# Performance work log

Measured on AMD Instinct MI355X. Metric: run time of the kernel, lower is better.

The kernel has to match this reference:

```python
import jax, jax.numpy as jnp
import numpy as np

B, T, F = 8, 1024, 80
STACK, STRIDE = 4, 4          # encoder.embed.right_context+1, subsampling_rate
G, E, C = 4, 16, 8192         # num_codebooks, embedding_dim, num_embeddings
DENC = 512                    # encoder.output_size()
TS = (T - STACK) // STRIDE + 1
FREG = 0.01                   # features_regularization_weight
EPS = 1e-5


def setup_inputs() -> dict:
    key = jax.random.key(0)
    ks = jax.random.split(key, 12)
    feats = jax.random.normal(ks[0], (B, T, F), jnp.float32)
    feats_lengths = jax.random.randint(ks[1], (B,), T // 2, T + 1, jnp.int32)
    # span masks (True = masked), mask_length=10 spans so full subsample windows get masked
    n_spans, ML = 16, 10
    starts = jax.random.randint(ks[2], (B, n_spans), 0, T - ML)
    pos = starts[:, :, None] + jnp.arange(ML)  # [B, n_spans, ML]
    masks = jnp.zeros((B, T), bool).at[jnp.arange(B)[:, None, None], pos].set(True)
    mask_emb = 0.1 * jax.random.normal(ks[3], (1, 1, F), jnp.float32)
    signal_mean = 0.1 * jax.random.normal(ks[4], (F,), jnp.float32)
    signal_istd = jax.random.uniform(ks[5], (F,), jnp.float32, 0.5, 1.5)
    projection = jax.random.normal(ks[6], (STACK * F, G * E), jnp.float32) * np.sqrt(2.0 / (STACK * F + G * E))
    embeddings = jax.random.normal(ks[7], (C, G, E), jnp.float32)
    encoder_top_n_out = 0.02 * jax.random.normal(ks[8], (G, DENC, C), jnp.float32)
    encoder_top_n_out_bias = jnp.zeros((G, C), jnp.float32)
    encoder_out = jax.random.normal(ks[9], (B, TS, DENC), jnp.float32)
    return {"feats": feats, "feats_lengths": feats_lengths, "masks": masks,
            "mask_emb": mask_emb, "signal_mean": signal_mean, "signal_istd": signal_istd,
            "projection": projection, "embeddings": embeddings,
            "encoder_top_n_out": encoder_top_n_out,
            "encoder_top_n_out_bias": encoder_top_n_out_bias,
            "encoder_out": encoder_out}


def _quantize_codes(latent, codebook):
    # latent: [N, G*E] -> codes [N, G]; codebook: [C, G, E]
    lat = latent.reshape(latent.shape[0], G, E)
    dist = (jnp.sum(lat ** 2, -1, keepdims=True)
            - 2.0 * jnp.einsum('ngd,cgd->ngc', lat, codebook)
            + jnp.sum(codebook ** 2, -1).T[None])  # [N, G, C]
    return jnp.argmin(dist, axis=-1)


def reference(feats, feats_lengths, masks, mask_emb, signal_mean, signal_istd,
              projection, embeddings, encoder_top_n_out, encoder_top_n_out_bias,
              encoder_out):
    # global CMVN
    xs = (feats - signal_mean) * signal_istd  # [B, T, F]
    features_pen = jnp.mean(xs ** 2)
    # masked signal (fed to the delegated encoder in the original; encoder_out stands in)
    _masked_xs = jnp.where(masks[:, :, None], mask_emb, xs)
    # unfold windows
    widx = jnp.arange(TS)[:, None] * STRIDE + jnp.arange(STACK)  # [TS, STACK]
    code_ids_mask = jnp.all(masks[:, widx], axis=2)  # [B, TS] (torch.min over bool window)
    stacked = xs[:, widx].reshape(B, TS, STACK * F)  # _stack_features on unmasked input
    # LayerNorm (no affine)
    mu = jnp.mean(stacked, -1, keepdims=True)
    var = jnp.var(stacked, -1, keepdims=True)
    normed = (stacked - mu) / jnp.sqrt(var + EPS)
    proj = normed @ projection  # [B, TS, G*E]
    target = _quantize_codes(proj.reshape(B * TS, G * E), embeddings).reshape(B, TS, G)
    # encoder output mask after subsampling
    lens_sub = jnp.maximum((feats_lengths - STACK) // STRIDE + 1, 0)
    out_mask = jnp.arange(TS)[None, :] < lens_sub[:, None]
    m = (out_mask & code_ids_mask).astype(jnp.float32)  # [B, TS]
    # big matmul: [B,1,TS,DENC] x [1,G,DENC,C] + bias -> [B,G,TS,C]
    logits = jnp.einsum('btd,gdc->bgtc', encoder_out, encoder_top_n_out) \
             + encoder_top_n_out_bias[None, :, None, :]
    logp = jax.nn.log_softmax(logits, axis=-1).transpose(0, 2, 1, 3)  # [B, TS, G, C]
    per = -jnp.take_along_axis(logp, target[..., None], axis=-1)[..., 0]  # [B, TS, G]
    denom = jnp.sum(m) + 1e-5
    loss = jnp.sum(per * m[:, :, None]) / (denom * G) + FREG * features_pen
    num_codes = jnp.sum(m) * G
    corr = (jnp.argmax(logits, -1).transpose(0, 2, 1) == target)
    codes_acc = jnp.sum(corr * m[:, :, None]) / num_codes
    vals = (target * m[:, :, None].astype(target.dtype)).reshape(-1)
    uniq_num_codes = jnp.zeros((C,), bool).at[vals].set(True).sum()
    return (loss, codes_acc, features_pen, num_codes, uniq_num_codes)
```

## Files before the change

kernel.cpp:

```cpp
#include <hip/hip_runtime.h>
#include <hip/hip_bf16.h>
#include <math.h>
#include <stddef.h>

#define NB 8
#define NT 1024
#define NF 80
#define NSTACK 4
#define NSTRIDE 4
#define NG 4
#define NE 16
#define NC 8192
#define ND 512
#define NTS 256
#define NP (NB*NTS)
#define SFD (NSTACK*NF)
#define FREG 0.01f
#define LNEPS 1e-5f

#define TCC 1024
#define CPT 4
#define PCH 16
#define PB 16

#define ROWS_MAX 2176
#define ROWCH 144
#define MT 9
#define QCH 16
#define QY 32
#define CT 128
#define QS 8
#define STG16H 1152
#define WST 1024

typedef __attribute__((ext_vector_type(8))) short short8;
typedef __attribute__((ext_vector_type(4))) float f32x4;

struct Ws {
  float penSum;
  unsigned int nA;
  unsigned int maskIsInt;
  unsigned int pad1;
  unsigned long long amax[NP*NG];
  float sumExp[NP*NG];
  float tLogit[NP*NG];
  int   targets[NP*NG];
  int   activeList[NP];
  float penPart[256];
  unsigned long long aminS[NP*NG*QS];
  float lat[NP][64];
  unsigned short aHiT[(size_t)(ND/8)*ROWS_MAX*8];
  unsigned short aLoT[(size_t)(ND/8)*ROWS_MAX*8];
  float part_se[NG][ROWS_MAX][CT];
  unsigned long long part_mx[NG][ROWS_MAX][CT];
};

__device__ inline unsigned short bf16_rne(float x) {
  unsigned u = __float_as_uint(x);
  unsigned r = u + 0x7FFFu + ((u >> 16) & 1u);
  return (unsigned short)(r >> 16);
}
__device__ inline unsigned fkey_asc(float d) {
  unsigned u = __float_as_uint(d);
  return (u & 0x80000000u) ? ~u : (u | 0x80000000u);
}
__device__ __forceinline__ void gload_lds16(const void* g, void* l) {
  __builtin_amdgcn_global_load_lds(
      (const __attribute__((address_space(1))) void*)g,
      (__attribute__((address_space(3))) void*)l, 16, 0, 0);
}

__global__ __launch_bounds__(256) void k_prologue(
    const float* __restrict__ feats, const float* __restrict__ mean,
    const float* __restrict__ istd, const unsigned char* __restrict__ m8,
    const int* __restrict__ lens, int doClear, Ws* ws) {
  const int tid = threadIdx.x;
  if (doClear) ws->aminS[(size_t)blockIdx.x*256 + tid] = ~0ull;

  const int N4 = NB*NT*NF/4;
  float s = 0.f;
  for (int i = blockIdx.x*256 + tid; i < N4; i += gridDim.x*256) {
    float4 v = reinterpret_cast<const float4*>(feats)[i];
    int f0 = (i*4) % NF;
    float x0 = (v.x - mean[f0+0]) * istd[f0+0];
    float x1 = (v.y - mean[f0+1]) * istd[f0+1];
    float x2 = (v.z - mean[f0+2]) * istd[f0+2];
    float x3 = (v.w - mean[f0+3]) * istd[f0+3];
    s += x0*x0 + x1*x1 + x2*x2 + x3*x3;
  }
  for (int o = 32; o; o >>= 1) s += __shfl_down(s, o);
  __shared__ float pr[4];
  if ((tid & 63) == 0) pr[tid >> 6] = s;
  __syncthreads();
  if (tid == 0) ws->penPart[blockIdx.x] = pr[0]+pr[1]+pr[2]+pr[3];

  if (blockIdx.x == 0) {
    __shared__ unsigned flag;
    __shared__ int sCnt[256];
    if (tid == 0) flag = 0;
    __syncthreads();
    unsigned nz = 0;
    int base = tid * 32;
    for (int i = base; i < base + 32; ++i)
      if ((i & 3) && m8[i]) nz = 1;
    if (nz) atomicOr(&flag, 1u);
    __syncthreads();
    bool isInt = (flag == 0);
    const int* m32 = (const int*)m8;

    unsigned bits = 0;
    int cnt = 0;
    #pragma unroll
    for (int j = 0; j < 8; ++j) {
      int p = tid*8 + j;
      int b = p >> 8, ts = p & (NTS-1);
      int t0 = b*NT + ts*NSTRIDE;
      bool allm;
      if (isInt) allm = m32[t0] && m32[t0+1] && m32[t0+2] && m32[t0+3];
      else       allm = m8[t0] && m8[t0+1] && m8[t0+2] && m8[t0+3];
      int ls = (lens[b] - NSTACK)/NSTRIDE + 1;
      if (ls < 0) ls = 0;
      bool act = allm && (ts < ls);
      bits |= (unsigned)act << j;
      cnt += act;
    }
    sCnt[tid] = cnt;
    __syncthreads();
    #pragma unroll
    for (int off = 1; off < 256; off <<= 1) {
      int v = (tid >= off) ? sCnt[tid - off] : 0;
      __syncthreads();
      sCnt[tid] += v;
      __syncthreads();
    }
    int wr = sCnt[tid] - cnt;
    #pragma unroll
    for (int j = 0; j < 8; ++j) {
      if (bits & (1u << j)) ws->activeList[wr++] = tid*8 + j;
    }
    if (tid == 255) ws->nA = (unsigned)sCnt[255];
  }
}

__global__ __launch_bounds__(256) void k_latprep(
    const float* __restrict__ feats, const float* __restrict__ mean,
    const float* __restrict__ istd, const float* __restrict__ projw,
    const float* __restrict__ enc, Ws* ws) {
  int nA = (int)ws->nA;
  int ai = blockIdx.x;
  int limit = ((nA + ROWCH - 1) / ROWCH) * ROWCH;
  int tid = threadIdx.x;

  if (ai >= nA) {
    if (ai < limit && tid < 64) {
      short8 z;
      #pragma unroll
      for (int j = 0; j < 8; ++j) z[j] = 0;
      *reinterpret_cast<short8*>(ws->aHiT + ((size_t)tid*ROWS_MAX + ai)*8) = z;
      *reinterpret_cast<short8*>(ws->aLoT + ((size_t)tid*ROWS_MAX + ai)*8) = z;
    }
    return;
  }

  int p = ws->activeList[ai];
  if (tid < 64) {
    const float* src = enc + (size_t)p*ND + tid*8;
    float4 x0 = *reinterpret_cast<const float4*>(src);
    float4 x1 = *reinterpret_cast<const float4*>(src + 4);
    float xv[8] = {x0.x, x0.y, x0.z, x0.w, x1.x, x1.y, x1.z, x1.w};
    short8 h, l;
    #pragma unroll
    for (int j = 0; j < 8; ++j) {
      unsigned short hi = bf16_rne(xv[j]);
      float rem = xv[j] - __uint_as_float((unsigned)hi << 16);
      h[j] = (short)hi;
      l[j] = (short)bf16_rne(rem);
    }
    *reinterpret_cast<short8*>(ws->aHiT + ((size_t)tid*ROWS_MAX + ai)*8) = h;
    *reinterpret_cast<short8*>(ws->aLoT + ((size_t)tid*ROWS_MAX + ai)*8) = l;
  }

  int b = p >> 8, ts = p & (NTS-1);
  __shared__ float sN[SFD];
  __shared__ float sPart[4*64];
  __shared__ float rS[4], rQ[4];

  for (int j = tid; j < SFD; j += 256) {
    int k = j / NF, f = j - k*NF;
    sN[j] = (feats[((size_t)b*NT + ts*NSTRIDE + k)*NF + f] - mean[f]) * istd[f];
  }
  __syncthreads();
  float s = 0.f, q = 0.f;
  for (int j = tid; j < SFD; j += 256) { float x = sN[j]; s += x; q += x*x; }
  for (int o = 32; o; o >>= 1) { s += __shfl_down(s, o); q += __shfl_down(q, o); }
  if ((tid & 63) == 0) { rS[tid>>6] = s; rQ[tid>>6] = q; }
  __syncthreads();
  float mu  = (rS[0]+rS[1]+rS[2]+rS[3]) * (1.f/SFD);
  float var = (rQ[0]+rQ[1]+rQ[2]+rQ[3]) * (1.f/SFD) - mu*mu;
  float inv = rsqrtf(var + LNEPS);
  for (int j = tid; j < SFD; j += 256) sN[j] = (sN[j]-mu)*inv;
  __syncthreads();
  {
    int j = tid & 63, part = tid >> 6;
    float a = 0.f;
    int i0 = part*80;
    for (int i = i0; i < i0+80; ++i) a = fmaf(sN[i], projw[i*64 + j], a);
    sPart[part*64 + j] = a;
  }
  __syncthreads();
  if (tid < 64)
    ws->lat[ai][tid] = sPart[tid] + sPart[64+tid] + sPart[128+tid] + sPart[192+tid];
}

__global__ __launch_bounds__(256) void k_qdist(const float* __restrict__ emb, Ws* ws) {
  int nA = (int)ws->nA;
  if (nA == 0) return;
  int tid = threadIdx.x;
  int g = tid >> 6, lane = tid & 63;
  int c = blockIdx.x * 64 + lane;
  int per = (nA + QY - 1) / QY;
  int a0 = blockIdx.y * per;
  int a1 = min(nA, a0 + per);
  int slot = blockIdx.x & (QS-1);

  const float4* e4 = reinterpret_cast<const float4*>(emb + ((size_t)c*NG + g)*NE);
  float4 b0 = e4[0], b1 = e4[1], b2 = e4[2], b3 = e4[3];
  float n2 = b0.x*b0.x + b0.y*b0.y + b0.z*b0.z + b0.w*b0.w
           + b1.x*b1.x + b1.y*b1.y + b1.z*b1.z + b1.w*b1.w
           + b2.x*b2.x + b2.y*b2.y + b2.z*b2.z + b2.w*b2.w
           + b3.x*b3.x + b3.y*b3.y + b3.z*b3.z + b3.w*b3.w;

  __shared__ float sL[QCH][64];
  for (int base = a0; base < a1; base += QCH) {
    int cnt = min(QCH, a1 - base);
    __syncthreads();
    for (int i = tid; i < cnt*64; i += 256)
      (&sL[0][0])[i] = (&ws->lat[0][0])[(size_t)(base + (i >> 6))*64 + (i & 63)];
    __syncthreads();
    for (int i = 0; i < cnt; ++i) {
      const float* lp = &sL[i][g*NE];
      float dot = lp[0]*b0.x + lp[1]*b0.y + lp[2]*b0.z + lp[3]*b0.w
                + lp[4]*b1.x + lp[5]*b1.y + lp[6]*b1.z + lp[7]*b1.w
                + lp[8]*b2.x + lp[9]*b2.y + lp[10]*b2.z + lp[11]*b2.w
                + lp[12]*b3.x + lp[13]*b3.y + lp[14]*b3.z + lp[15]*b3.w;
      float d = n2 - 2.f*dot;
      float mv = d; int mc = c;
      #pragma unroll
      for (int off = 32; off; off >>= 1) {
        float ov = __shfl_xor(mv, off);
        int   oc = __shfl_xor(mc, off);
        if (ov < mv || (ov == mv && oc < mc)) { mv = ov; mc = oc; }
      }
      if (lane == 0) {
        unsigned long long key =
            ((unsigned long long)fkey_asc(mv) << 32) | (unsigned)mc;
        atomicMin(&ws->aminS[(size_t)((base + i)*NG + g)*QS + slot], key);
      }
    }
  }
}

__global__ __launch_bounds__(512, 4) void k_logits_mfma(
    const float* __restrict__ W, const float* __restrict__ bias, Ws* ws) {
  const int nA = (int)ws->nA;
  if (nA == 0) return;
  const int nCh = (nA + ROWCH - 1) / ROWCH;
  const int tid = threadIdx.x;
  const int wave = tid >> 6, lane = tid & 63;
  const int sub = wave & 3, kh = wave >> 2;
  const int g = blockIdx.y;
  const int c0blk = blockIdx.x * 64;
  const int c0w = c0blk + sub * 16;
  const int lo16 = lane & 15, hi4 = lane >> 4;
  const int cOut0 = c0w + hi4*4;
  float bv[4];
  #pragma unroll
  for (int v = 0; v < 4; ++v) bv[v] = bias[g*NC + cOut0 + v];

  __shared__ __align__(16) unsigned char smem[53248];
  unsigned short* sH = (unsigned short*)smem;
  unsigned short* sLb = (unsigned short*)(smem + 18432);
  float* sW = (float*)(smem + 36864);
  f32x4 (*sAcc)[MT][64] = (f32x4 (*)[MT][64])smem;
  float (*sEs)[ROWCH] = (float (*)[ROWCH])(smem + 36864);
  unsigned long long (*sMx)[ROWCH] =
      (unsigned long long (*)[ROWCH])(smem + 36864 + 2560);

  const int krow0 = tid >> 4,       woff0 = (tid & 15) * 4;
  const int krow1 = (tid+512) >> 4, woff1 = ((tid+512) & 15) * 4;
  const size_t wk0 = (size_t)((krow0 < 32) ? krow0 : 224 + krow0);
  const size_t wk1 = (size_t)((krow1 < 32) ? krow1 : 224 + krow1);
  const float* __restrict__ wG = W + ((size_t)g*ND)*NC + c0blk;

  const int wRd = (kh*32 + hi4*8)*64 + sub*16 + lo16;

  for (int ch = 0; ch < nCh; ++ch) {
    const int r0 = ch * ROWCH;

    size_t off0, off1, off2; bool v2;
    {
      int t = tid;
      int part = t/144, row = t - part*144;
      off0 = ((size_t)((part>>2)*32 + (part&3))*ROWS_MAX + r0 + row)*8;
      t = tid + 512;
      part = t/144; row = t - part*144;
      off1 = ((size_t)((part>>2)*32 + (part&3))*ROWS_MAX + r0 + row)*8;
      t = tid + 1024;
      v2 = (t < STG16H);
      part = t/144; row = t - part*144;
      off2 = v2 ? ((size_t)((part>>2)*32 + (part&3))*ROWS_MAX + r0 + row)*8 : 0;
    }

    f32x4 acc[MT];
    #pragma unroll
    for (int mt = 0; mt < MT; ++mt) acc[mt] = (f32x4){0.f, 0.f, 0.f, 0.f};

    gload_lds16(ws->aHiT + off0, sH + (size_t)tid*8);
    gload_lds16(ws->aHiT + off1, sH + (size_t)(tid + 512)*8);
    if (v2) gload_lds16(ws->aHiT + off2, sH + (size_t)(tid + 1024)*8);
    gload_lds16(wG + wk0*NC + woff0, sW + (size_t)tid*4);
    gload_lds16(wG + wk1*NC + woff1, sW + (size_t)(tid + 512)*4);
    __syncthreads();

    #pragma unroll 1
    for (int step = 0; step < 8; ++step) {
      const size_t kAdv = (size_t)step*4*ROWS_MAX*8;
      gload_lds16(ws->aLoT + off0 + kAdv, sLb + (size_t)tid*8);
      gload_lds16(ws->aLoT + off1 + kAdv, sLb + (size_t)(tid + 512)*8);
      if (v2) gload_lds16(ws->aLoT + off2 + kAdv, sLb + (size_t)(tid + 1024)*8);
      float wv[8];
      #pragma unroll
      for (int j = 0; j < 8; ++j) wv[j] = sW[wRd + j*64];
      short8 whi, wlo;
      #pragma unroll
      for (int j = 0; j < 8; ++j) {
        unsigned short h = bf16_rne(wv[j]);
        float rem = wv[j] - __uint_as_float((unsigned)h << 16);
        whi[j] = (short)h;
        wlo[j] = (short)bf16_rne(rem);
      }
      const unsigned short* bpH = sH + ((size_t)((kh*4 + hi4)*144 + lo16))*8;
      #pragma unroll
      for (int mt = 0; mt < MT; ++mt) {
        short8 bh = *reinterpret_cast<const short8*>(bpH + mt*128);
        acc[mt] = __builtin_amdgcn_mfma_f32_16x16x32_bf16(whi, bh, acc[mt], 0, 0, 0);
        acc[mt] = __builtin_amdgcn_mfma_f32_16x16x32_bf16(wlo, bh, acc[mt], 0, 0, 0);
      }
      __syncthreads();
      if (step < 7) {
        const size_t kAdv2 = kAdv + (size_t)4*ROWS_MAX*8;
        gload_lds16(ws->aHiT + off0 + kAdv2, sH + (size_t)tid*8);
        gload_lds16(ws->aHiT + off1 + kAdv2, sH + (size_t)(tid + 512)*8);
        if (v2) gload_lds16(ws->aHiT + off2 + kAdv2, sH + (size_t)(tid + 1024)*8);
        const size_t wAdv = (size_t)(step+1)*32*NC;
        gload_lds16(wG + (wk0*NC + wAdv) + woff0, sW + (size_t)tid*4);
        gload_lds16(wG + (wk1*NC + wAdv) + woff1, sW + (size_t)(tid + 512)*4);
      }
      const unsigned short* bpL = sLb + ((size_t)((kh*4 + hi4)*144 + lo16))*8;
      #pragma unroll
      for (int mt = 0; mt < MT; ++mt) {
        short8 bl = *reinterpret_cast<const short8*>(bpL + mt*128);
        acc[mt] = __builtin_amdgcn_mfma_f32_16x16x32_bf16(whi, bl, acc[mt], 0, 0, 0);
      }
      __syncthreads();
    }

    if (kh == 1) {
      #pragma unroll
      for (int mt = 0; mt < MT; ++mt) sAcc[sub][mt][lane] = acc[mt];
    }
    __syncthreads();

    if (kh == 0) {
      #pragma unroll
      for (int mt = 0; mt < MT; ++mt) {
        const int row = r0 + mt*16 + lo16;
        int tgt = -1;
        if (row < nA) {
          const unsigned long long* ap = ws->aminS + (size_t)(row*NG + g)*QS;
          unsigned long long m = ap[0];
          #pragma unroll
          for (int s2 = 1; s2 < QS; ++s2) {
            unsigned long long v = ap[s2];
            if (v < m) m = v;
          }
          tgt = (int)(unsigned)(m & 0xFFFFFFFFull);
          if (blockIdx.x == 0 && wave == 0 && hi4 == 0)
            ws->targets[row*NG + g] = tgt;
        }
        f32x4 oth = sAcc[sub][mt][lane];
        float lv[4];
        #pragma unroll
        for (int v = 0; v < 4; ++v) lv[v] = (acc[mt][v] + oth[v]) + bv[v];
        #pragma unroll
        for (int v = 0; v < 4; ++v)
          if (tgt == cOut0 + v) ws->tLogit[row*NG + g] = lv[v];
        float es = expf(lv[0]) + expf(lv[1]) + expf(lv[2]) + expf(lv[3]);
        float mv = lv[0]; int mi = cOut0;
        if (lv[1] > mv) { mv = lv[1]; mi = cOut0+1; }
        if (lv[2] > mv) { mv = lv[2]; mi = cOut0+2; }
        if (lv[3] > mv) { mv = lv[3]; mi = cOut0+3; }
        #pragma unroll
        for (int off = 16; off <= 32; off <<= 1) {
          es += __shfl_xor(es, off);
          float ov = __shfl_xor(mv, off);
          int   oi = __shfl_xor(mi, off);
          if (ov > mv || (ov == mv && oi < mi)) { mv = ov; mi = oi; }
        }
        if (hi4 == 0) {
          sEs[sub][mt*16 + lo16] = es;
          unsigned key = __float_as_uint(mv);
          key = (key & 0x80000000u) ? ~key : (key | 0x80000000u);
          sMx[sub][mt*16 + lo16] = ((unsigned long long)key << 32)
                                 | (unsigned long long)(0xFFFFFFFFu - (unsigned)mi);
        }
      }
    }
    __syncthreads();
    if (tid < ROWCH) {
      float e = sEs[0][tid] + sEs[1][tid] + sEs[2][tid] + sEs[3][tid];
      unsigned long long m0 = sMx[0][tid], m1 = sMx[1][tid];
      unsigned long long m2 = sMx[2][tid], m3 = sMx[3][tid];
      unsigned long long ma = m0 > m1 ? m0 : m1;
      unsigned long long mb = m2 > m3 ? m2 : m3;
      unsigned long long mx = ma > mb ? ma : mb;
      int grow = r0 + tid;
      ws->part_se[g][grow][blockIdx.x] = e;
      ws->part_mx[g][grow][blockIdx.x] = mx;
    }
    __syncthreads();
  }
}

__global__ __launch_bounds__(256) void k_red_l(Ws* ws) {
  int nA = (int)ws->nA;
  int pair = blockIdx.x*4 + (threadIdx.x >> 6);
  int lane = threadIdx.x & 63;
  int row = pair >> 2, g = pair & 3;
  if (row >= nA) return;
  float e = ws->part_se[g][row][lane] + ws->part_se[g][row][lane + 64];
  unsigned long long a = ws->part_mx[g][row][lane];
  unsigned long long b = ws->part_mx[g][row][lane + 64];
  unsigned long long mx = a > b ? a : b;
  #pragma unroll
  for (int off = 32; off; off >>= 1) {
    e += __shfl_xor(e, off);
    unsigned long long o = __shfl_xor(mx, off);
    if (o > mx) mx = o;
  }
  if (lane == 0) {
    ws->sumExp[row*NG + g] = e;
    ws->amax[row*NG + g] = mx;
  }
}

__global__ __launch_bounds__(256) void k_quant(
    const float* __restrict__ feats, const float* __restrict__ mean,
    const float* __restrict__ istd, const float* __restrict__ projw,
    const float* __restrict__ emb, Ws* ws) {
  if (blockIdx.x >= ws->nA) return;
  int ai = blockIdx.x;
  int p = ws->activeList[ai];
  int b = p >> 8, ts = p & (NTS-1);
  int tid = threadIdx.x;
  __shared__ float sN[SFD];
  __shared__ float sPart[4*64];
  __shared__ float sLat[NG*NE];
  __shared__ float sRedS[256];
  __shared__ int   sRedC[256];
  __shared__ float rS[4], rQ[4];
  __shared__ int   sTgt[NG];

  for (int j = tid; j < SFD; j += 256) {
    int k = j / NF, f = j - k*NF;
    sN[j] = (feats[((size_t)b*NT + ts*NSTRIDE + k)*NF + f] - mean[f]) * istd[f];
  }
  __syncthreads();
  float s = 0.f, q = 0.f;
  for (int j = tid; j < SFD; j += 256) { float x = sN[j]; s += x; q += x*x; }
  for (int o = 32; o; o >>= 1) { s += __shfl_down(s, o); q += __shfl_down(q, o); }
  if ((tid & 63) == 0) { rS[tid>>6] = s; rQ[tid>>6] = q; }
  __syncthreads();
  float mu  = (rS[0]+rS[1]+rS[2]+rS[3]) * (1.f/SFD);
  float var = (rQ[0]+rQ[1]+rQ[2]+rQ[3]) * (1.f/SFD) - mu*mu;
  float inv = rsqrtf(var + LNEPS);
  for (int j = tid; j < SFD; j += 256) sN[j] = (sN[j]-mu)*inv;
  __syncthreads();
  {
    int j = tid & 63, part = tid >> 6;
    float a = 0.f;
    int i0 = part*80;
    for (int i = i0; i < i0+80; ++i) a = fmaf(sN[i], projw[i*64 + j], a);
    sPart[part*64 + j] = a;
  }
  __syncthreads();
  if (tid < 64) sLat[tid] = sPart[tid] + sPart[64+tid] + sPart[128+tid] + sPart[192+tid];
  __syncthreads();

  for (int gg = 0; gg < NG; ++gg) {
    float lg[NE];
    #pragma unroll
    for (int e = 0; e < NE; ++e) lg[e] = sLat[gg*NE + e];
    float best = 3.4e38f; int bc = NC;
    for (int c = tid; c < NC; c += 256) {
      const float4* cb4 = reinterpret_cast<const float4*>(emb + ((size_t)c*NG + gg)*NE);
      float4 a0 = cb4[0], a1 = cb4[1], a2 = cb4[2], a3 = cb4[3];
      float dot = 0.f, n2 = 0.f;
      dot = fmaf(lg[0],  a0.x, dot); n2 = fmaf(a0.x, a0.x, n2);
      dot = fmaf(lg[1],  a0.y, dot); n2 = fmaf(a0.y, a0.y, n2);
      dot = fmaf(lg[2],  a0.z, dot); n2 = fmaf(a0.z, a0.z, n2);
      dot = fmaf(lg[3],  a0.w, dot); n2 = fmaf(a0.w, a0.w, n2);
      dot = fmaf(lg[4],  a1.x, dot); n2 = fmaf(a1.x, a1.x, n2);
      dot = fmaf(lg[5],  a1.y, dot); n2 = fmaf(a1.y, a1.y, n2);
      dot = fmaf(lg[6],  a1.z, dot); n2 = fmaf(a1.z, a1.z, n2);
      dot = fmaf(lg[7],  a1.w, dot); n2 = fmaf(a1.w, a1.w, n2);
      dot = fmaf(lg[8],  a2.x, dot); n2 = fmaf(a2.x, a2.x, n2);
      dot = fmaf(lg[9],  a2.y, dot); n2 = fmaf(a2.y, a2.y, n2);
      dot = fmaf(lg[10], a2.z, dot); n2 = fmaf(a2.z, a2.z, n2);
      dot = fmaf(lg[11], a2.w, dot); n2 = fmaf(a2.w, a2.w, n2);
      dot = fmaf(lg[12], a3.x, dot); n2 = fmaf(a3.x, a3.x, n2);
      dot = fmaf(lg[13], a3.y, dot); n2 = fmaf(a3.y, a3.y, n2);
      dot = fmaf(lg[14], a3.z, dot); n2 = fmaf(a3.z, a3.z, n2);
      dot = fmaf(lg[15], a3.w, dot); n2 = fmaf(a3.w, a3.w, n2);
      float sc = n2 - 2.f*dot;
      if (sc < best) { best = sc; bc = c; }
    }
    sRedS[tid] = best; sRedC[tid] = bc;
    __syncthreads();
    for (int off = 128; off; off >>= 1) {
      if (tid < off) {
        float os = sRedS[tid+off]; int oc = sRedC[tid+off];
        if (os < sRedS[tid] || (os == sRedS[tid] && oc < sRedC[tid])) {
          sRedS[tid] = os; sRedC[tid] = oc;
        }
      }
      __syncthreads();
    }
    if (tid == 0) sTgt[gg] = sRedC[0];
    __syncthreads();
  }
  if (tid < NG) ws->targets[ai*NG + tid] = sTgt[tid];
}

__global__ __launch_bounds__(256) void k_logits(
    const float* __restrict__ W, const float* __restrict__ bias,
    const float* __restrict__ enc, Ws* ws) {
  const int nA = (int)ws->nA;
  if (nA == 0) return;
  const int nCh = (nA + PCH - 1) / PCH;
  const int g = blockIdx.y;
  const int cbase = blockIdx.x * TCC + threadIdx.x * CPT;
  const float* __restrict__ Wg = W + (size_t)g*ND*NC;
  const float b0 = bias[g*NC + cbase + 0];
  const float b1 = bias[g*NC + cbase + 1];
  const float b2 = bias[g*NC + cbase + 2];
  const float b3 = bias[g*NC + cbase + 3];
  __shared__ float4 sEnc[PCH][ND/4];
  __shared__ int sP[PCH];

  for (int ch = blockIdx.z; ch < nCh; ch += PB) {
    if (threadIdx.x < PCH) {
      int ai = ch*PCH + threadIdx.x;
      sP[threadIdx.x] = (ai < nA) ? ws->activeList[ai] : -1;
    }
    __syncthreads();
    for (int i = threadIdx.x; i < PCH*(ND/4); i += 256) {
      int qq = i >> 7, r = i & 127;
      int p = sP[qq];
      sEnc[qq][r] = (p >= 0) ? reinterpret_cast<const float4*>(enc)[p*(ND/4) + r]
                             : make_float4(0.f, 0.f, 0.f, 0.f);
    }
    __syncthreads();

    float acc[PCH][CPT];
    #pragma unroll
    for (int qq = 0; qq < PCH; ++qq)
      #pragma unroll
      for (int j = 0; j < CPT; ++j) acc[qq][j] = 0.f;
    for (int d = 0; d < ND; d += 4) {
      const float* wp = Wg + (size_t)d*NC + cbase;
      float4 w0 = *reinterpret_cast<const float4*>(wp);
      float4 w1 = *reinterpret_cast<const float4*>(wp + NC);
      float4 w2 = *reinterpret_cast<const float4*>(wp + 2*NC);
      float4 w3 = *reinterpret_cast<const float4*>(wp + 3*NC);
      int dq = d >> 2;
      #pragma unroll
      for (int qq = 0; qq < PCH; ++qq) {
        float4 e = sEnc[qq][dq];
        acc[qq][0] = fmaf(e.x, w0.x, acc[qq][0]);
        acc[qq][1] = fmaf(e.x, w0.y, acc[qq][1]);
        acc[qq][2] = fmaf(e.x, w0.z, acc[qq][2]);
        acc[qq][3] = fmaf(e.x, w0.w, acc[qq][3]);
        acc[qq][0] = fmaf(e.y, w1.x, acc[qq][0]);
        acc[qq][1] = fmaf(e.y, w1.y, acc[qq][1]);
        acc[qq][2] = fmaf(e.y, w1.z, acc[qq][2]);
        acc[qq][3] = fmaf(e.y, w1.w, acc[qq][3]);
        acc[qq][0] = fmaf(e.z, w2.x, acc[qq][0]);
        acc[qq][1] = fmaf(e.z, w2.y, acc[qq][1]);
        acc[qq][2] = fmaf(e.z, w2.z, acc[qq][2]);
        acc[qq][3] = fmaf(e.z, w2.w, acc[qq][3]);
        acc[qq][0] = fmaf(e.w, w3.x, acc[qq][0]);
        acc[qq][1] = fmaf(e.w, w3.y, acc[qq][1]);
        acc[qq][2] = fmaf(e.w, w3.z, acc[qq][2]);
        acc[qq][3] = fmaf(e.w, w3.w, acc[qq][3]);
      }
    }

    #pragma unroll
    for (int qq = 0; qq < PCH; ++qq) {
      int ai = ch*PCH + qq;
      if (ai < nA) {
        float l0 = acc[qq][0] + b0;
        float l1 = acc[qq][1] + b1;
        float l2 = acc[qq][2] + b2;
        float l3 = acc[qq][3] + b3;
        int tgt = ws->targets[ai*NG + g];
        if ((unsigned)(tgt - cbase) < (unsigned)CPT) {
          float tv = (tgt == cbase) ? l0 : (tgt == cbase+1) ? l1
                   : (tgt == cbase+2) ? l2 : l3;
          ws->tLogit[ai*NG + g] = tv;
        }
        float es = expf(l0) + expf(l1) + expf(l2) + expf(l3);
        float mv = l0; int mi = cbase;
        if (l1 > mv) { mv = l1; mi = cbase+1; }
        if (l2 > mv) { mv = l2; mi = cbase+2; }
        if (l3 > mv) { mv = l3; mi = cbase+3; }
        for (int o = 32; o; o >>= 1) {
          es += __shfl_down(es, o);
          float ov = __shfl_down(mv, o);
          int   oi = __shfl_down(mi, o);
          if (ov > mv || (ov == mv && oi < mi)) { mv = ov; mi = oi; }
        }
        if ((threadIdx.x & 63) == 0) {
          atomicAdd(&ws->sumExp[ai*NG + g], es);
          unsigned key = __float_as_uint(mv);
          key = (key & 0x80000000u) ? ~key : (key | 0x80000000u);
          unsigned long long pk =
              ((unsigned long long)key << 32) |
              (unsigned long long)(0xFFFFFFFFu - (unsigned)mi);
          atomicMax(&ws->amax[ai*NG + g], pk);
        }
      }
    }
    __syncthreads();
  }
}

__global__ __launch_bounds__(256) void k_final(Ws* ws, float* __restrict__ out) {
  int tid = threadIdx.x;
  int nA = (int)ws->nA;
  __shared__ unsigned sbm[NC/32];
  sbm[tid] = 0u;
  __syncthreads();

  float sumPer = 0.f, sumCorr = 0.f;
  for (int i = tid; i < nA*NG; i += 256) {
    int tgt = ws->targets[i];
    sumPer += logf(ws->sumExp[i]) - ws->tLogit[i];
    unsigned long long pk = ws->amax[i];
    int mi = (int)(0xFFFFFFFFu - (unsigned)(pk & 0xFFFFFFFFull));
    if (mi == tgt) sumCorr += 1.f;
    atomicOr(&sbm[tgt >> 5], 1u << (tgt & 31));
  }
  __syncthreads();
  unsigned w = sbm[tid];
  if (tid == 0 && nA < NP) w |= 1u;
  int uniq = __popc(w);
  float pen1 = ws->penPart[tid];

  __shared__ float rs[4], rc[4], rp[4]; __shared__ int ru[4];
  float s1 = sumPer, s2 = sumCorr, s4 = pen1; int s3 = uniq;
  for (int o = 32; o; o >>= 1) {
    s1 += __shfl_down(s1, o);
    s2 += __shfl_down(s2, o);
    s3 += __shfl_down(s3, o);
    s4 += __shfl_down(s4, o);
  }
  if ((tid & 63) == 0) { rs[tid>>6] = s1; rc[tid>>6] = s2; ru[tid>>6] = s3; rp[tid>>6] = s4; }
  __syncthreads();
  if (tid == 0) {
    float sp = rs[0]+rs[1]+rs[2]+rs[3];
    float sc = rc[0]+rc[1]+rc[2]+rc[3];
    int   un = ru[0]+ru[1]+ru[2]+ru[3];
    float ps = rp[0]+rp[1]+rp[2]+rp[3];
    float pen   = ps / (float)(NB*NT*NF);
    float denom = (float)nA + 1e-5f;
    float nc    = (float)(nA * NG);
    out[0] = sp / (denom * (float)NG) + FREG * pen;
    out[1] = sc / nc;
    out[2] = pen;
    out[3] = nc;
    out[4] = (float)un;
  }
}

extern "C" void kernel_launch(void* const* d_in, const int* in_sizes, int n_in,
                              void* d_out, int out_size, void* d_ws, size_t ws_size,
                              hipStream_t stream) {
  const float* feats = (const float*)d_in[0];
  const int*   lens  = (const int*)d_in[1];
  const unsigned char* masks = (const unsigned char*)d_in[2];
  const float* mean  = (const float*)d_in[4];
  const float* istd  = (const float*)d_in[5];
  const float* projw = (const float*)d_in[6];
  const float* emb   = (const float*)d_in[7];
  const float* W     = (const float*)d_in[8];
  const float* bias  = (const float*)d_in[9];
  const float* enc   = (const float*)d_in[10];
  Ws* ws = (Ws*)d_ws;
  float* out = (float*)d_out;

  bool big = ws_size >= sizeof(Ws);
  if (big) {
    k_prologue<<<256, 256, 0, stream>>>(feats, mean, istd, masks, lens, 1, ws);
    k_latprep<<<ROWS_MAX, 256, 0, stream>>>(feats, mean, istd, projw, enc, ws);
    k_qdist<<<dim3(NC/64, QY), 256, 0, stream>>>(emb, ws);
    k_logits_mfma<<<dim3(CT, NG), 512, 0, stream>>>(W, bias, ws);
    k_red_l<<<NP, 256, 0, stream>>>(ws);
  } else {
    size_t zr = offsetof(Ws, aminS);
    hipMemsetAsync(d_ws, 0, ws_size < zr ? ws_size : zr, stream);
    k_prologue<<<256, 256, 0, stream>>>(feats, mean, istd, masks, lens, 0, ws);
    k_quant<<<NP, 256, 0, stream>>>(feats, mean, istd, projw, emb, ws);
    k_logits<<<dim3(NC/TCC, NG, PB), 256, 0, stream>>>(W, bias, enc, ws);
  }
  k_final<<<1, 256, 0, stream>>>(ws, out);
}
```

Measured before the change: 75.14 us.

## Fuse row reduction and final loss into logits kernel via last-block atomics

Removes the separate k_red_l and k_final launches on the big-workspace path. The last logits block finishing each codebook group, found with an atomic counter, reduces the partial sum-exp and max values for that group. The last group to finish then computes the final loss, accuracy, penalty and unique-code outputs. This saves two kernel launches and their gaps, but puts the reduction on a few serial blocks and depends on threadfence and atomic-counter ordering, with counters reset in the prologue.

```diff
diff --git a/kernel.cpp b/kernel.cpp
--- a/kernel.cpp
+++ b/kernel.cpp
@@ -31,7 +31,6 @@
 #define CT 128
 #define QS 8
 #define STG16H 1152
-#define WST 1024
 
 typedef __attribute__((ext_vector_type(8))) short short8;
 typedef __attribute__((ext_vector_type(4))) float f32x4;
@@ -47,6 +46,9 @@
   int   targets[NP*NG];
   int   activeList[NP];
   float penPart[256];
+  unsigned int redCnt[NG];
+  unsigned int finCnt;
+  unsigned int pad2[3];
   unsigned long long aminS[NP*NG*QS];
   float lat[NP][64];
   unsigned short aHiT[(size_t)(ND/8)*ROWS_MAX*8];
@@ -95,6 +97,11 @@
   if (tid == 0) ws->penPart[blockIdx.x] = pr[0]+pr[1]+pr[2]+pr[3];
 
   if (blockIdx.x == 0) {
+    if (tid == 0) {
+      ws->redCnt[0] = 0u; ws->redCnt[1] = 0u;
+      ws->redCnt[2] = 0u; ws->redCnt[3] = 0u;
+      ws->finCnt = 0u;
+    }
     __shared__ unsigned flag;
     __shared__ int sCnt[256];
     if (tid == 0) flag = 0;
@@ -261,7 +268,8 @@
 }
 
 __global__ __launch_bounds__(512, 4) void k_logits_mfma(
-    const float* __restrict__ W, const float* __restrict__ bias, Ws* ws) {
+    const float* __restrict__ W, const float* __restrict__ bias, Ws* ws,
+    float* __restrict__ out) {
   const int nA = (int)ws->nA;
   if (nA == 0) return;
   const int nCh = (nA + ROWCH - 1) / ROWCH;
@@ -278,6 +286,7 @@
   for (int v = 0; v < 4; ++v) bv[v] = bias[g*NC + cOut0 + v];
 
   __shared__ __align__(16) unsigned char smem[53248];
+  __shared__ unsigned sFlag, sFin;
   unsigned short* sH = (unsigned short*)smem;
   unsigned short* sLb = (unsigned short*)(smem + 18432);
   float* sW = (float*)(smem + 36864);
@@ -291,7 +300,6 @@
   const size_t wk0 = (size_t)((krow0 < 32) ? krow0 : 224 + krow0);
   const size_t wk1 = (size_t)((krow1 < 32) ? krow1 : 224 + krow1);
   const float* __restrict__ wG = W + ((size_t)g*ND)*NC + c0blk;
-
   const int wRd = (kh*32 + hi4*8)*64 + sub*16 + lo16;
 
   for (int ch = 0; ch < nCh; ++ch) {
@@ -430,27 +438,86 @@
     }
     __syncthreads();
   }
-}
-
-__global__ __launch_bounds__(256) void k_red_l(Ws* ws) {
-  int nA = (int)ws->nA;
-  int pair = blockIdx.x*4 + (threadIdx.x >> 6);
-  int lane = threadIdx.x & 63;
-  int row = pair >> 2, g = pair & 3;
-  if (row >= nA) return;
-  float e = ws->part_se[g][row][lane] + ws->part_se[g][row][lane + 64];
-  unsigned long long a = ws->part_mx[g][row][lane];
-  unsigned long long b = ws->part_mx[g][row][lane + 64];
-  unsigned long long mx = a > b ? a : b;
-  #pragma unroll
-  for (int off = 32; off; off >>= 1) {
-    e += __shfl_xor(e, off);
-    unsigned long long o = __shfl_xor(mx, off);
-    if (o > mx) mx = o;
-  }
-  if (lane == 0) {
-    ws->sumExp[row*NG + g] = e;
-    ws->amax[row*NG + g] = mx;
+
+  if (tid == 0) {
+    __threadfence();
+    sFlag = atomicAdd(&ws->redCnt[g], 1u);
+  }
+  __syncthreads();
+  if (sFlag != CT-1) return;
+  __threadfence();
+
+  for (int row = wave; row < nA; row += 8) {
+    float e = ws->part_se[g][row][lane] + ws->part_se[g][row][lane + 64];
+    unsigned long long a = ws->part_mx[g][row][lane];
+    unsigned long long b = ws->part_mx[g][row][lane + 64];
+    unsigned long long mx = a > b ? a : b;
+    #pragma unroll
+    for (int off = 32; off; off >>= 1) {
+      e += __shfl_xor(e, off);
+      unsigned long long o = __shfl_xor(mx, off);
+      if (o > mx) mx = o;
+    }
+    if (lane == 0) {
+      ws->sumExp[row*NG + g] = e;
+      ws->amax[row*NG + g] = mx;
+    }
+  }
+
+  if (tid == 0) {
+    __threadfence();
+    sFin = atomicAdd(&ws->finCnt, 1u);
+  }
+  __syncthreads();
+  if (sFin != NG-1) return;
+  __threadfence();
+
+  {
+    unsigned* sbm = (unsigned*)smem;
+    float* rS1 = (float*)(smem + 2048);
+    float* rS2 = rS1 + 8;
+    float* rS4 = rS2 + 8;
+    int*   rS3 = (int*)(rS4 + 8);
+    if (tid < 256) sbm[tid] = 0u;
+    __syncthreads();
+    float sumPer = 0.f, sumCorr = 0.f;
+    for (int i = tid; i < nA*NG; i += 512) {
+      int tgt = ws->targets[i];
+      sumPer += logf(ws->sumExp[i]) - ws->tLogit[i];
+      unsigned long long pk = ws->amax[i];
+      int mi = (int)(0xFFFFFFFFu - (unsigned)(pk & 0xFFFFFFFFull));
+      if (mi == tgt) sumCorr += 1.f;
+      atomicOr(&sbm[tgt >> 5], 1u << (tgt & 31));
+    }
+    float pen1 = (tid < 256) ? ws->penPart[tid] : 0.f;
+    __syncthreads();
+    unsigned wbits = (tid < 256) ? sbm[tid] : 0u;
+    if (tid == 0 && nA < NP) wbits |= 1u;
+    int uniq = __popc(wbits);
+    float s1 = sumPer, s2 = sumCorr, s4 = pen1; int s3 = uniq;
+    for (int o = 32; o; o >>= 1) {
+      s1 += __shfl_down(s1, o);
+      s2 += __shfl_down(s2, o);
+      s3 += __shfl_down(s3, o);
+      s4 += __shfl_down(s4, o);
+    }
+    if (lane == 0) { rS1[wave] = s1; rS2[wave] = s2; rS3[wave] = s3; rS4[wave] = s4; }
+    __syncthreads();
+    if (tid == 0) {
+      float sp = 0.f, sc = 0.f, ps = 0.f; int un = 0;
+      #pragma unroll
+      for (int wv = 0; wv < 8; ++wv) {
+        sp += rS1[wv]; sc += rS2[wv]; un += rS3[wv]; ps += rS4[wv];
+      }
+      float pen   = ps / (float)(NB*NT*NF);
+      float denom = (float)nA + 1e-5f;
+      float nc    = (float)(nA * NG);
+      out[0] = sp / (denom * (float)NG) + FREG * pen;
+      out[1] = sc / nc;
+      out[2] = pen;
+      out[3] = nc;
+      out[4] = (float)un;
+    }
   }
 }
 
@@ -715,14 +782,13 @@
     k_prologue<<<256, 256, 0, stream>>>(feats, mean, istd, masks, lens, 1, ws);
     k_latprep<<<ROWS_MAX, 256, 0, stream>>>(feats, mean, istd, projw, enc, ws);
     k_qdist<<<dim3(NC/64, QY), 256, 0, stream>>>(emb, ws);
-    k_logits_mfma<<<dim3(CT, NG), 512, 0, stream>>>(W, bias, ws);
-    k_red_l<<<NP, 256, 0, stream>>>(ws);
+    k_logits_mfma<<<dim3(CT, NG), 512, 0, stream>>>(W, bias, ws, out);
   } else {
     size_t zr = offsetof(Ws, aminS);
     hipMemsetAsync(d_ws, 0, ws_size < zr ? ws_size : zr, stream);
     k_prologue<<<256, 256, 0, stream>>>(feats, mean, istd, masks, lens, 0, ws);
     k_quant<<<NP, 256, 0, stream>>>(feats, mean, istd, projw, emb, ws);
     k_logits<<<dim3(NC/TCC, NG, PB), 256, 0, stream>>>(W, bias, enc, ws);
-  }
-  k_final<<<1, 256, 0, stream>>>(ws, out);
-}
+    k_final<<<1, 256, 0, stream>>>(ws, out);
+  }
+}
```

After: 107.0 us. 1.42x slower.
